# Kernel optimization log

Measured on AMD Instinct MI355X. Metric: run time of the kernel, lower is better.

Reference implementation:

```python
import jax, jax.numpy as jnp
import numpy as np

B, C, N = 16, 64, 2048
K, KS, OC = 20, 20, 64
BN_EPS = 1e-5


def setup_inputs() -> dict:
    key = jax.random.key(0)
    k1, k2, k3, k4 = jax.random.split(key, 4)
    feature = jax.random.normal(k1, (B, C, N), dtype=jnp.float32)
    neigh_indexs = jax.random.randint(k2, (B * N, K), 0, B * N, dtype=jnp.int64)
    permatrix = jax.random.normal(k3, (B * N, K, KS), dtype=jnp.float32)
    conv_w = jax.random.normal(k4, (OC, 2 * C), dtype=jnp.float32) * 0.05  # 1x1 conv weight
    conv_b = jnp.zeros((OC,), dtype=jnp.float32)
    gamma = jnp.ones((OC,), dtype=jnp.float32)
    beta = jnp.zeros((OC,), dtype=jnp.float32)
    return {"feature": feature, "neigh_indexs": neigh_indexs, "permatrix": permatrix,
            "conv_w": conv_w, "conv_b": conv_b, "gamma": gamma, "beta": beta}


def _forward(feature, neigh_indexs, permatrix, conv_w, conv_b, gamma, beta):
    bsize, num_feat, num_pts = feature.shape
    # [B, C, N] -> [B*N, C]
    flat = jnp.transpose(feature, (0, 2, 1)).reshape(bsize * num_pts, num_feat)
    # neighbor gather: [B*N, K, C] -> [B*N, C, K]
    feats = jnp.transpose(flat[neigh_indexs], (0, 2, 1))
    f_repeat = jnp.broadcast_to(feats[:, :, 0:1], feats.shape)
    f_relative = feats - f_repeat
    feats = jnp.concatenate([f_repeat, f_relative], axis=1)  # [B*N, 2C, K]
    # per-point small matmul with permutation matrix: [B*N, 2C, KS]
    feats = jnp.einsum('nck,nks->ncs', feats, permatrix)
    # 1x1 conv over channel dim: [B*N, OC, KS]
    out = jnp.einsum('ncs,oc->nos', feats, conv_w) + conv_b[None, :, None]
    # max over neighbors, reshape to [B, OC, N]
    out = jnp.max(out, axis=-1).reshape(bsize, num_pts, -1)
    out = jnp.transpose(out, (0, 2, 1))  # [B, OC, N]
    # BatchNorm1d (training-mode forward: biased var over batch & points)
    mean = jnp.mean(out, axis=(0, 2), keepdims=True)
    var = jnp.var(out, axis=(0, 2), keepdims=True)
    out = (out - mean) * jax.lax.rsqrt(var + BN_EPS)
    return out * gamma[None, :, None] + beta[None, :, None]


def reference(feature, neigh_indexs, permatrix, conv_w, conv_b, gamma, beta):
    return _forward(feature, neigh_indexs, permatrix, conv_w, conv_b, gamma, beta)
```

## Files before the change

### kernel.cpp

```cpp
#include <hip/hip_runtime.h>

#define B_   16
#define C_   64
#define N_   2048
#define M_   (B_ * N_)
#define K_   20
#define KS_  20
#define OC_  64
#define NWAVE2 8192

__global__ __launch_bounds__(256) void k_project(
    const float* __restrict__ feat,
    const float* __restrict__ conv_w,
    float* __restrict__ pq)
{
    const int lane = threadIdx.x & 63;
    const int wg   = blockIdx.x * 4 + (threadIdx.x >> 6);
    float w2[64], wd[64];
    const float4* cw4 = (const float4*)conv_w;
    #pragma unroll
    for (int j = 0; j < 16; ++j) {
        float4 a = cw4[lane * 32 + j];
        float4 b = cw4[lane * 32 + 16 + j];
        w2[4*j+0] = b.x; w2[4*j+1] = b.y; w2[4*j+2] = b.z; w2[4*j+3] = b.w;
        wd[4*j+0] = a.x - b.x; wd[4*j+1] = a.y - b.y;
        wd[4*j+2] = a.z - b.z; wd[4*j+3] = a.w - b.w;
    }
    const int m0 = wg * 16;
    int b0 = m0 >> 11, p0 = m0 & 2047;
    float fv = feat[((size_t)(b0 * 64 + lane)) * 2048 + p0];
    for (int mi = 0; mi < 16; ++mi) {
        const int m = m0 + mi;
        float fnext = 0.f;
        if (mi < 15) {
            const int mn = m + 1;
            fnext = feat[((size_t)((mn >> 11) * 64 + lane)) * 2048 + (mn & 2047)];
        }
        float accP = 0.f, accQ = 0.f;
        #pragma unroll
        for (int c = 0; c < 64; ++c) {
            float fc = __int_as_float(
                __builtin_amdgcn_readlane(__float_as_int(fv), c));
            accP = fmaf(w2[c], fc, accP);
            accQ = fmaf(wd[c], fc, accQ);
        }
        pq[(size_t)m * 128 + lane]      = accP;
        pq[(size_t)m * 128 + 64 + lane] = accQ;
        fv = fnext;
    }
}

__global__ __launch_bounds__(256) void k_points(
    const float* __restrict__ pq,
    const int*   __restrict__ nidx,
    const float* __restrict__ perm,
    const float* __restrict__ conv_b,
    float* __restrict__ pre,
    float* __restrict__ partials)
{
    const int lane = threadIdx.x & 63;
    const int wg = __builtin_amdgcn_readfirstlane(
        (int)(blockIdx.x * 4 + (threadIdx.x >> 6)));
    const float bias = conv_b[lane];
    float sum = 0.f, sumsq = 0.f;
    for (int it = 0; it < 4; ++it) {
        const int n = wg + NWAVE2 * it;
        const int*   __restrict__ ip = nidx + (size_t)n * K_;
        const float* __restrict__ pp = perm + (size_t)n * (K_ * KS_);
        float pk[20];
        #pragma unroll
        for (int k = 0; k < 20; ++k) {
            const int ik = ip[k];
            pk[k] = pq[(size_t)ik * 128 + lane];
        }
        const float q = pq[(size_t)ip[0] * 128 + 64 + lane];
        #pragma unroll
        for (int k = 0; k < 20; ++k) pk[k] += q;
        float acc[20];
        #pragma unroll
        for (int s = 0; s < 20; ++s) acc[s] = bias;
        #pragma unroll
        for (int k = 0; k < 20; ++k) {
            #pragma unroll
            for (int s = 0; s < 20; ++s)
                acc[s] = fmaf(pk[k], pp[k * 20 + s], acc[s]);
        }
        float mv = acc[0];
        #pragma unroll
        for (int s = 1; s < 20; ++s) mv = fmaxf(mv, acc[s]);
        pre[(size_t)n * 64 + lane] = mv;
        sum += mv;
        sumsq = fmaf(mv, mv, sumsq);
    }
    partials[(size_t)wg * 128 + lane]      = sum;
    partials[(size_t)wg * 128 + 64 + lane] = sumsq;
}

__global__ __launch_bounds__(256) void k_stats(
    const float* __restrict__ partials,
    const float* __restrict__ gamma,
    const float* __restrict__ beta,
    float* __restrict__ stats)
{
    const int ch  = blockIdx.x;
    const int tid = threadIdx.x;
    double s = 0.0, s2 = 0.0;
    for (int w = tid; w < NWAVE2; w += 256) {
        s  += (double)partials[(size_t)w * 128 + ch];
        s2 += (double)partials[(size_t)w * 128 + 64 + ch];
    }
    __shared__ double sh_s[256];
    __shared__ double sh_q[256];
    sh_s[tid] = s; sh_q[tid] = s2;
    __syncthreads();
    for (int off = 128; off > 0; off >>= 1) {
        if (tid < off) { sh_s[tid] += sh_s[tid + off]; sh_q[tid] += sh_q[tid + off]; }
        __syncthreads();
    }
    if (tid == 0) {
        const double inv_n = 1.0 / (double)M_;
        double mean = sh_s[0] * inv_n;
        double var  = sh_q[0] * inv_n - mean * mean;
        double inv  = 1.0 / sqrt(var + 1e-5);
        double sc   = (double)gamma[ch] * inv;
        stats[ch]      = (float)sc;
        stats[64 + ch] = (float)((double)beta[ch] - mean * sc);
    }
}

__global__ __launch_bounds__(256) void k_apply(
    const float* __restrict__ pre,
    const float* __restrict__ stats,
    float* __restrict__ out)
{
    __shared__ float tile[64 * 65];
    __shared__ float scl[64];
    __shared__ float shf[64];
    const int tid = threadIdx.x;
    if (tid < 64)       scl[tid]      = stats[tid];
    else if (tid < 128) shf[tid - 64] = stats[tid];
    __syncthreads();
    const int b  = blockIdx.x >> 5;
    const int pt = (blockIdx.x & 31) * 64;
    const int c  = tid & 63;
    const int r0 = tid >> 6;
    #pragma unroll
    for (int i = 0; i < 16; ++i) {
        const int r = i * 4 + r0;
        float v = pre[((size_t)(b * 2048 + pt + r)) * 64 + c];
        tile[c * 65 + r] = fmaf(v, scl[c], shf[c]);
    }
    __syncthreads();
    #pragma unroll
    for (int i = 0; i < 16; ++i) {
        const int o = i * 4 + r0;
        out[((size_t)(b * 64 + o)) * 2048 + pt + c] = tile[o * 65 + c];
    }
}

extern "C" void kernel_launch(void* const* d_in, const int* in_sizes, int n_in,
                              void* d_out, int out_size, void* d_ws, size_t ws_size,
                              hipStream_t stream) {
    const float* feat   = (const float*)d_in[0];
    const int*   nidx   = (const int*)  d_in[1];
    const float* perm   = (const float*)d_in[2];
    const float* conv_w = (const float*)d_in[3];
    const float* conv_b = (const float*)d_in[4];
    const float* gamma  = (const float*)d_in[5];
    const float* beta   = (const float*)d_in[6];
    float* out = (float*)d_out;

    char* ws = (char*)d_ws;
    float* pq       = (float*)ws;
    float* pre      = (float*)(ws + (size_t)M_ * 128 * 4);
    float* partials = (float*)(ws + (size_t)M_ * 128 * 4
                                  + (size_t)M_ * 64 * 4);
    float* stats    = (float*)(ws + (size_t)M_ * 128 * 4
                                  + (size_t)M_ * 64 * 4
                                  + (size_t)NWAVE2 * 128 * 4);

    hipLaunchKernelGGL(k_project, dim3(512),  dim3(256), 0, stream, feat, conv_w, pq);
    hipLaunchKernelGGL(k_points,  dim3(2048), dim3(256), 0, stream, pq, nidx, perm,
                       conv_b, pre, partials);
    hipLaunchKernelGGL(k_stats,   dim3(64),   dim3(256), 0, stream, partials, gamma,
                       beta, stats);
    hipLaunchKernelGGL(k_apply,   dim3(512),  dim3(256), 0, stream, pre, stats, out);
}
```

Measured before the change: 195.9 us.

## Double-buffer permatrix into LDS via async global_load_lds and prefetch indices

The per-point kernel now stages each point's 20x20 permutation matrix into a per-wave double buffer in LDS using direct global-to-LDS loads. The next point's matrix and neighbour indices are prefetched while the current point's gathers and FMAs run. Neighbour indices are loaded once per wave and broadcast with readlane instead of scalar loads. The projection kernel also splits its channel reduction into two independent accumulator chains for more ILP. The manual waitcnt encodings are fragile and the extra LDS use may reduce occupancy.

```diff
diff --git a/kernel.cpp b/kernel.cpp
--- a/kernel.cpp
+++ b/kernel.cpp
@@ -8,6 +8,12 @@
 #define KS_  20
 #define OC_  64
 #define NWAVE2 8192
+
+__device__ __forceinline__ void load_lds16(const float* g, float* l) {
+    __builtin_amdgcn_global_load_lds(
+        (const __attribute__((address_space(1))) void*)g,
+        (__attribute__((address_space(3))) void*)l, 16, 0, 0);
+}
 
 __global__ __launch_bounds__(256) void k_project(
     const float* __restrict__ feat,
@@ -36,16 +42,20 @@
             const int mn = m + 1;
             fnext = feat[((size_t)((mn >> 11) * 64 + lane)) * 2048 + (mn & 2047)];
         }
-        float accP = 0.f, accQ = 0.f;
-        #pragma unroll
-        for (int c = 0; c < 64; ++c) {
-            float fc = __int_as_float(
+        float p0a = 0.f, p1a = 0.f, q0a = 0.f, q1a = 0.f;
+        #pragma unroll
+        for (int c = 0; c < 32; ++c) {
+            float f0 = __int_as_float(
                 __builtin_amdgcn_readlane(__float_as_int(fv), c));
-            accP = fmaf(w2[c], fc, accP);
-            accQ = fmaf(wd[c], fc, accQ);
-        }
-        pq[(size_t)m * 128 + lane]      = accP;
-        pq[(size_t)m * 128 + 64 + lane] = accQ;
+            float f1 = __int_as_float(
+                __builtin_amdgcn_readlane(__float_as_int(fv), c + 32));
+            p0a = fmaf(w2[c], f0, p0a);
+            p1a = fmaf(w2[c + 32], f1, p1a);
+            q0a = fmaf(wd[c], f0, q0a);
+            q1a = fmaf(wd[c + 32], f1, q1a);
+        }
+        pq[(size_t)m * 128 + lane]      = p0a + p1a;
+        pq[(size_t)m * 128 + 64 + lane] = q0a + q1a;
         fv = fnext;
     }
 }
@@ -58,32 +68,65 @@
     float* __restrict__ pre,
     float* __restrict__ partials)
 {
-    const int lane = threadIdx.x & 63;
-    const int wg = __builtin_amdgcn_readfirstlane(
-        (int)(blockIdx.x * 4 + (threadIdx.x >> 6)));
+    __shared__ float plds[4 * 2 * 400];
+    const int tid  = threadIdx.x;
+    const int lane = tid & 63;
+    const int w    = __builtin_amdgcn_readfirstlane(tid >> 6);
+    const int wg   = __builtin_amdgcn_readfirstlane((int)blockIdx.x * 4 + w);
+    float* mybuf = &plds[w * 800];
+
     const float bias = conv_b[lane];
     float sum = 0.f, sumsq = 0.f;
+
+    {
+        const float* src = perm + (size_t)wg * 400;
+        load_lds16(src + lane * 4, mybuf);
+        if (lane < 36) load_lds16(src + 256 + lane * 4, mybuf + 256);
+    }
+    int iv = 0;
+    if (lane < 20) iv = nidx[(size_t)wg * K_ + lane];
+
+    #pragma unroll
     for (int it = 0; it < 4; ++it) {
         const int n = wg + NWAVE2 * it;
-        const int*   __restrict__ ip = nidx + (size_t)n * K_;
-        const float* __restrict__ pp = perm + (size_t)n * (K_ * KS_);
+        float* cur = mybuf + (it & 1) * 400;
+        int ik[20];
+        #pragma unroll
+        for (int k = 0; k < 20; ++k) ik[k] = __builtin_amdgcn_readlane(iv, k);
+        float q = pq[(size_t)ik[0] * 128 + 64 + lane];
         float pk[20];
         #pragma unroll
+        for (int k = 0; k < 20; ++k) pk[k] = pq[(size_t)ik[k] * 128 + lane];
+        if (it < 3) {
+            const int nn = n + NWAVE2;
+            if (lane < 20) iv = nidx[(size_t)nn * K_ + lane];
+            const float* src = perm + (size_t)nn * 400;
+            float* nxt = mybuf + ((it + 1) & 1) * 400;
+            load_lds16(src + lane * 4, nxt);
+            if (lane < 36) load_lds16(src + 256 + lane * 4, nxt + 256);
+        }
+        if (it < 3) __builtin_amdgcn_s_waitcnt(0x0F74);
+        else        __builtin_amdgcn_s_waitcnt(0x0F70);
+        __asm__ volatile("" ::: "memory");
+
+        float acc[20];
+        #pragma unroll
+        for (int s = 0; s < 20; ++s) acc[s] = bias;
+        #pragma unroll
         for (int k = 0; k < 20; ++k) {
-            const int ik = ip[k];
-            pk[k] = pq[(size_t)ik * 128 + lane];
-        }
-        const float q = pq[(size_t)ip[0] * 128 + 64 + lane];
-        #pragma unroll
-        for (int k = 0; k < 20; ++k) pk[k] += q;
-        float acc[20];
-        #pragma unroll
-        for (int s = 0; s < 20; ++s) acc[s] = bias;
-        #pragma unroll
-        for (int k = 0; k < 20; ++k) {
-            #pragma unroll
-            for (int s = 0; s < 20; ++s)
-                acc[s] = fmaf(pk[k], pp[k * 20 + s], acc[s]);
+            const float t = pk[k] + q;
+            const float4* pr = (const float4*)(cur + k * 20);
+            float4 a0 = pr[0], a1 = pr[1], a2 = pr[2], a3 = pr[3], a4 = pr[4];
+            acc[ 0] = fmaf(t, a0.x, acc[ 0]); acc[ 1] = fmaf(t, a0.y, acc[ 1]);
+            acc[ 2] = fmaf(t, a0.z, acc[ 2]); acc[ 3] = fmaf(t, a0.w, acc[ 3]);
+            acc[ 4] = fmaf(t, a1.x, acc[ 4]); acc[ 5] = fmaf(t, a1.y, acc[ 5]);
+            acc[ 6] = fmaf(t, a1.z, acc[ 6]); acc[ 7] = fmaf(t, a1.w, acc[ 7]);
+            acc[ 8] = fmaf(t, a2.x, acc[ 8]); acc[ 9] = fmaf(t, a2.y, acc[ 9]);
+            acc[10] = fmaf(t, a2.z, acc[10]); acc[11] = fmaf(t, a2.w, acc[11]);
+            acc[12] = fmaf(t, a3.x, acc[12]); acc[13] = fmaf(t, a3.y, acc[13]);
+            acc[14] = fmaf(t, a3.z, acc[14]); acc[15] = fmaf(t, a3.w, acc[15]);
+            acc[16] = fmaf(t, a4.x, acc[16]); acc[17] = fmaf(t, a4.y, acc[17]);
+            acc[18] = fmaf(t, a4.z, acc[18]); acc[19] = fmaf(t, a4.w, acc[19]);
         }
         float mv = acc[0];
         #pragma unroll
```

Result: faster. 176.9 us (-9.7%).

## Restructure point kernel: 4 points per wave, LDS-staged perm, split reductions

Applied to the files above, without the earlier changes.

The point kernel now handles four points per wave, with each lane computing four output channels for one point. The permutation matrices are staged into LDS with coalesced float4 loads, and the next neighbor row is prefetched from pq while the current one is used in the FMAs. The BN stats reduction is split into a two-stage float/double tree reduction that reuses the pq buffer as scratch. The projection kernel uses twice as many waves and two independent accumulator chains per output. The changes trade higher register pressure (80 accumulators per lane) for fewer redundant global loads of perm.

```diff
diff --git a/kernel.cpp b/kernel.cpp
--- a/kernel.cpp
+++ b/kernel.cpp
@@ -7,7 +7,7 @@
 #define K_   20
 #define KS_  20
 #define OC_  64
-#define NWAVE2 8192
+#define NW2  8192
 
 __global__ __launch_bounds__(256) void k_project(
     const float* __restrict__ feat,
@@ -26,26 +26,30 @@
         wd[4*j+0] = a.x - b.x; wd[4*j+1] = a.y - b.y;
         wd[4*j+2] = a.z - b.z; wd[4*j+3] = a.w - b.w;
     }
-    const int m0 = wg * 16;
+    const int m0 = wg * 8;
     int b0 = m0 >> 11, p0 = m0 & 2047;
     float fv = feat[((size_t)(b0 * 64 + lane)) * 2048 + p0];
-    for (int mi = 0; mi < 16; ++mi) {
+    for (int mi = 0; mi < 8; ++mi) {
         const int m = m0 + mi;
         float fnext = 0.f;
-        if (mi < 15) {
+        if (mi < 7) {
             const int mn = m + 1;
             fnext = feat[((size_t)((mn >> 11) * 64 + lane)) * 2048 + (mn & 2047)];
         }
-        float accP = 0.f, accQ = 0.f;
+        float p0a = 0.f, p1a = 0.f, q0a = 0.f, q1a = 0.f;
         #pragma unroll
-        for (int c = 0; c < 64; ++c) {
-            float fc = __int_as_float(
+        for (int c = 0; c < 32; ++c) {
+            float f0 = __int_as_float(
                 __builtin_amdgcn_readlane(__float_as_int(fv), c));
-            accP = fmaf(w2[c], fc, accP);
-            accQ = fmaf(wd[c], fc, accQ);
-        }
-        pq[(size_t)m * 128 + lane]      = accP;
-        pq[(size_t)m * 128 + 64 + lane] = accQ;
+            float f1 = __int_as_float(
+                __builtin_amdgcn_readlane(__float_as_int(fv), c + 32));
+            p0a = fmaf(w2[c], f0, p0a);
+            p1a = fmaf(w2[c + 32], f1, p1a);
+            q0a = fmaf(wd[c], f0, q0a);
+            q1a = fmaf(wd[c + 32], f1, q1a);
+        }
+        pq[(size_t)m * 128 + lane]      = p0a + p1a;
+        pq[(size_t)m * 128 + 64 + lane] = q0a + q1a;
         fv = fnext;
     }
 }
@@ -58,73 +62,140 @@
     float* __restrict__ pre,
     float* __restrict__ partials)
 {
-    const int lane = threadIdx.x & 63;
-    const int wg = __builtin_amdgcn_readfirstlane(
-        (int)(blockIdx.x * 4 + (threadIdx.x >> 6)));
-    const float bias = conv_b[lane];
-    float sum = 0.f, sumsq = 0.f;
-    for (int it = 0; it < 4; ++it) {
-        const int n = wg + NWAVE2 * it;
-        const int*   __restrict__ ip = nidx + (size_t)n * K_;
-        const float* __restrict__ pp = perm + (size_t)n * (K_ * KS_);
-        float pk[20];
+    __shared__ __align__(16) float plds[4 * 4 * 404];
+    const int tid  = threadIdx.x;
+    const int lane = tid & 63;
+    const int og   = lane & 15;
+    const int p    = lane >> 4;
+    const int wv   = tid >> 6;
+    const int wg   = (int)blockIdx.x * 4 + wv;
+    const int nb   = wg * 4;
+    const int n    = nb + p;
+    float* wbuf = &plds[wv * 1616];
+
+    int2 iv2 = make_int2(0, 0);
+    if (lane < 40) iv2 = ((const int2*)(nidx + (size_t)nb * 20))[lane];
+
+    #pragma unroll
+    for (int pp = 0; pp < 4; ++pp) {
+        const float4* src = (const float4*)(perm + (size_t)(nb + pp) * 400);
+        float* dst = wbuf + pp * 404;
+        float4 v0 = src[lane];
+        *(float4*)(dst + lane * 4) = v0;
+        if (lane < 36) {
+            float4 v1 = src[64 + lane];
+            *(float4*)(dst + 256 + lane * 4) = v1;
+        }
+    }
+
+    const float4 bias = *(const float4*)(conv_b + og * 4);
+
+    int ik0 = __shfl(iv2.x, p * 10);
+    const float* pqb = pq + (size_t)ik0 * 128 + og * 4;
+    float4 q4  = *(const float4*)(pqb + 64);
+    float4 pkc = *(const float4*)(pqb);
+
+    __syncthreads();
+
+    float acc[4][20];
+    #pragma unroll
+    for (int s = 0; s < 20; ++s) {
+        acc[0][s] = bias.x; acc[1][s] = bias.y;
+        acc[2][s] = bias.z; acc[3][s] = bias.w;
+    }
+
+    const float* gbase = wbuf + p * 404;
+    #pragma unroll
+    for (int k = 0; k < 20; ++k) {
+        float4 pkn = pkc;
+        if (k < 19) {
+            const int kk = k + 1;
+            int src = p * 10 + (kk >> 1);
+            int ikn = (kk & 1) ? __shfl(iv2.y, src) : __shfl(iv2.x, src);
+            pkn = *(const float4*)(pq + (size_t)ikn * 128 + og * 4);
+        }
+        float t[4];
+        t[0] = pkc.x + q4.x; t[1] = pkc.y + q4.y;
+        t[2] = pkc.z + q4.z; t[3] = pkc.w + q4.w;
         #pragma unroll
-        for (int k = 0; k < 20; ++k) {
-            const int ik = ip[k];
-            pk[k] = pq[(size_t)ik * 128 + lane];
-        }
-        const float q = pq[(size_t)ip[0] * 128 + 64 + lane];
+        for (int c = 0; c < 5; ++c) {
+            float4 m4 = *(const float4*)(gbase + k * 20 + c * 4);
+            #pragma unroll
+            for (int j = 0; j < 4; ++j) {
+                acc[j][c*4+0] = fmaf(t[j], m4.x, acc[j][c*4+0]);
+                acc[j][c*4+1] = fmaf(t[j], m4.y, acc[j][c*4+1]);
+                acc[j][c*4+2] = fmaf(t[j], m4.z, acc[j][c*4+2]);
+                acc[j][c*4+3] = fmaf(t[j], m4.w, acc[j][c*4+3]);
+            }
+        }
+        pkc = pkn;
+    }
+
+    float mv[4];
+    #pragma unroll
+    for (int j = 0; j < 4; ++j) {
+        float m = acc[j][0];
         #pragma unroll
-        for (int k = 0; k < 20; ++k) pk[k] += q;
-        float acc[20];
-        #pragma unroll
-        for (int s = 0; s < 20; ++s) acc[s] = bias;
-        #pragma unroll
-        for (int k = 0; k < 20; ++k) {
-            #pragma unroll
-            for (int s = 0; s < 20; ++s)
-                acc[s] = fmaf(pk[k], pp[k * 20 + s], acc[s]);
-        }
-        float mv = acc[0];
-        #pragma unroll
-        for (int s = 1; s < 20; ++s) mv = fmaxf(mv, acc[s]);
-        pre[(size_t)n * 64 + lane] = mv;
-        sum += mv;
-        sumsq = fmaf(mv, mv, sumsq);
-    }
-    partials[(size_t)wg * 128 + lane]      = sum;
-    partials[(size_t)wg * 128 + 64 + lane] = sumsq;
-}
-
-__global__ __launch_bounds__(256) void k_stats(
+        for (int s = 1; s < 20; ++s) m = fmaxf(m, acc[j][s]);
+        mv[j] = m;
+    }
+    *(float4*)(pre + (size_t)n * 64 + og * 4) = make_float4(mv[0], mv[1], mv[2], mv[3]);
+
+    float sv[4], sw[4];
+    #pragma unroll
+    for (int j = 0; j < 4; ++j) {
+        float v = mv[j], w = mv[j] * mv[j];
+        v += __shfl_xor(v, 16); v += __shfl_xor(v, 32);
+        w += __shfl_xor(w, 16); w += __shfl_xor(w, 32);
+        sv[j] = v; sw[j] = w;
+    }
+    if (lane < 16) {
+        *(float4*)(partials + (size_t)wg * 128 + lane * 4)
+            = make_float4(sv[0], sv[1], sv[2], sv[3]);
+        *(float4*)(partials + (size_t)wg * 128 + 64 + lane * 4)
+            = make_float4(sw[0], sw[1], sw[2], sw[3]);
+    }
+}
+
+__global__ __launch_bounds__(256) void k_red1(
     const float* __restrict__ partials,
+    float* __restrict__ mid)
+{
+    const int t = threadIdx.x;
+    const int c = t & 127, rh = t >> 7;
+    const float* base = partials + (size_t)blockIdx.x * 64 * 128;
+    float s = 0.f;
+    for (int i = rh; i < 64; i += 2) s += base[(size_t)i * 128 + c];
+    __shared__ float sh[256];
+    sh[t] = s;
+    __syncthreads();
+    if (t < 128) mid[(size_t)blockIdx.x * 128 + t] = sh[t] + sh[t + 128];
+}
+
+__global__ __launch_bounds__(256) void k_red2(
+    const float* __restrict__ mid,
     const float* __restrict__ gamma,
     const float* __restrict__ beta,
     float* __restrict__ stats)
 {
-    const int ch  = blockIdx.x;
-    const int tid = threadIdx.x;
-    double s = 0.0, s2 = 0.0;
-    for (int w = tid; w < NWAVE2; w += 256) {
-        s  += (double)partials[(size_t)w * 128 + ch];
-        s2 += (double)partials[(size_t)w * 128 + 64 + ch];
-    }
-    __shared__ double sh_s[256];
-    __shared__ double sh_q[256];
-    sh_s[tid] = s; sh_q[tid] = s2;
-    __syncthreads();
-    for (int off = 128; off > 0; off >>= 1) {
-        if (tid < off) { sh_s[tid] += sh_s[tid + off]; sh_q[tid] += sh_q[tid + off]; }
-        __syncthreads();
-    }
-    if (tid == 0) {
+    const int t = threadIdx.x;
+    const int c = t & 127, rh = t >> 7;
+    double s = 0.0;
+    for (int i = rh; i < 128; i += 2) s += (double)mid[(size_t)i * 128 + c];
+    __shared__ double shd[256];
+    __shared__ double tot[128];
+    shd[t] = s;
+    __syncthreads();
+    if (t < 128) tot[t] = shd[t] + shd[t + 128];
+    __syncthreads();
+    if (t < 64) {
         const double inv_n = 1.0 / (double)M_;
-        double mean = sh_s[0] * inv_n;
-        double var  = sh_q[0] * inv_n - mean * mean;
+        double mean = tot[t] * inv_n;
+        double var  = tot[t + 64] * inv_n - mean * mean;
         double inv  = 1.0 / sqrt(var + 1e-5);
-        double sc   = (double)gamma[ch] * inv;
-        stats[ch]      = (float)sc;
-        stats[64 + ch] = (float)((double)beta[ch] - mean * sc);
+        double sc   = (double)gamma[t] * inv;
+        stats[t]      = (float)sc;
+        stats[64 + t] = (float)((double)beta[t] - mean * sc);
     }
 }
 
@@ -171,18 +242,18 @@
     float* out = (float*)d_out;
 
     char* ws = (char*)d_ws;
-    float* pq       = (float*)ws;
-    float* pre      = (float*)(ws + (size_t)M_ * 128 * 4);
-    float* partials = (float*)(ws + (size_t)M_ * 128 * 4
-                                  + (size_t)M_ * 64 * 4);
-    float* stats    = (float*)(ws + (size_t)M_ * 128 * 4
-                                  + (size_t)M_ * 64 * 4
-                                  + (size_t)NWAVE2 * 128 * 4);
-
-    hipLaunchKernelGGL(k_project, dim3(512),  dim3(256), 0, stream, feat, conv_w, pq);
+    size_t off = 0;
+    float* pq       = (float*)(ws + off); off += (size_t)M_ * 128 * 4;
+    float* pre      = (float*)(ws + off); off += (size_t)M_ * 64 * 4;
+    float* partials = (float*)(ws + off); off += (size_t)NW2 * 128 * 4;
+    float* mid      = pq;
+    float* stats    = pq + 128 * 128;
+
+    hipLaunchKernelGGL(k_project, dim3(1024), dim3(256), 0, stream, feat, conv_w, pq);
     hipLaunchKernelGGL(k_points,  dim3(2048), dim3(256), 0, stream, pq, nidx, perm,
                        conv_b, pre, partials);
-    hipLaunchKernelGGL(k_stats,   dim3(64),   dim3(256), 0, stream, partials, gamma,
+    hipLaunchKernelGGL(k_red1,    dim3(128),  dim3(256), 0, stream, partials, mid);
+    hipLaunchKernelGGL(k_red2,    dim3(1),    dim3(256), 0, stream, mid, gamma,
                        beta, stats);
     hipLaunchKernelGGL(k_apply,   dim3(512),  dim3(256), 0, stream, pre, stats, out);
 }
```

Result: faster. 185.4 us (-5.4%).
